# Kernel tuning notes

Hardware: AMD Instinct MI355X
Metric: run time of the kernel (lower is better)

The kernel has to match this reference:

```python
import jax, jax.numpy as jnp
import numpy as np

N_NODES = 50000
N_EDGES = 800000
IN_FEATS = 128
HIDDEN = 256
N_CLASSES = 64


def setup_inputs() -> dict:
    key = jax.random.key(0)
    ks = jax.random.split(key, 16)
    def w(k, shape, fan_in):
        return jax.random.normal(k, shape, dtype=jnp.float32) * (1.0 / np.sqrt(fan_in))
    inp = {
        "x": jax.random.normal(ks[0], (N_NODES, IN_FEATS), dtype=jnp.float32),
        "edge_src": jax.random.randint(ks[1], (N_EDGES,), 0, N_NODES, dtype=jnp.int32),
        "edge_dst": jax.random.randint(ks[2], (N_EDGES,), 0, N_NODES, dtype=jnp.int32),
        # layer 0: in_feats -> hidden
        "W0s": w(ks[3], (IN_FEATS, HIDDEN), IN_FEATS),
        "W0n": w(ks[4], (IN_FEATS, HIDDEN), IN_FEATS),
        "b0": jnp.zeros((HIDDEN,), dtype=jnp.float32),
        # layer 1: hidden -> hidden
        "W1s": w(ks[5], (HIDDEN, HIDDEN), HIDDEN),
        "W1n": w(ks[6], (HIDDEN, HIDDEN), HIDDEN),
        "b1": jnp.zeros((HIDDEN,), dtype=jnp.float32),
        # layer 2: hidden -> hidden (last conv also outputs hidden per source code)
        "W2s": w(ks[7], (HIDDEN, HIDDEN), HIDDEN),
        "W2n": w(ks[8], (HIDDEN, HIDDEN), HIDDEN),
        "b2": jnp.zeros((HIDDEN,), dtype=jnp.float32),
        # fc1: hidden -> n_classes
        "Wfc": w(ks[9], (HIDDEN, N_CLASSES), HIDDEN),
        "bfc": jnp.zeros((N_CLASSES,), dtype=jnp.float32),
    }
    return inp


def _sage_layer(h, src, dst, Ws, Wn, b):
    # mean-neighbor aggregation: segment-sum messages, divide by in-degree
    msg = h[src]  # [E, D] irregular gather
    agg = jax.ops.segment_sum(msg, dst, num_segments=N_NODES)  # [N, D]
    deg = jax.ops.segment_sum(jnp.ones_like(dst, dtype=h.dtype), dst, num_segments=N_NODES)
    h_neigh = agg / jnp.maximum(deg, 1.0)[:, None]
    # DGL SAGEConv (mean): fc_self(h) + fc_neigh(h_neigh) + bias
    return h @ Ws + h_neigh @ Wn + b


def reference(x, edge_src, edge_dst, W0s, W0n, b0, W1s, W1n, b1, W2s, W2n, b2, Wfc, bfc):
    # forward applies dropout (identity at eval) and NO activation between layers,
    # matching the original module's forward().
    h = _sage_layer(x, edge_src, edge_dst, W0s, W0n, b0)
    h = _sage_layer(h, edge_src, edge_dst, W1s, W1n, b1)
    h = _sage_layer(h, edge_src, edge_dst, W2s, W2n, b2)
    return h @ Wfc + bfc  # [N, n_classes]
```

## Files before the change

### kernel.cpp

```cpp
#include <hip/hip_runtime.h>

#define NN 50000
#define NE 800000
#define NE_HALF 400000
#define F_IN 128
#define HID 256
#define N_CLS 64
#define SCAN_BLOCKS ((NN + 255) / 256)
#define HEPT 4
#define HB2 ((NE + 256 * HEPT - 1) / (256 * HEPT))
#define HBH ((NE_HALF + 256 * HEPT - 1) / (256 * HEPT))
#define CF_BLOCKS 36
#define CL_BLOCKS 9
#define GA_BLOCKS ((NN + 127) / 128)
#define CROWS 515

typedef _Float16 half8 __attribute__((ext_vector_type(8)));
typedef float f32x4 __attribute__((ext_vector_type(4)));

__device__ __forceinline__ const float* virtC1_row(int r, const float* W0s,
                                                   const float* W0n, const float* b0) {
    if (r < 0) return nullptr;
    if (r < 128) return W0s + (size_t)r * 256;
    if (r < 256) return W0n + (size_t)(r - 128) * 256;
    if (r == 512) return b0;
    return nullptr;
}

__device__ __forceinline__ int shift_src(int r) {
    if (r >= 128 && r < 512) return r - 128;
    if (r == 513) return 512;
    if (r == 514) return 513;
    return -1;
}

__device__ __forceinline__ void compose_first_dev(
    int bx, const float* __restrict__ W0s, const float* __restrict__ W0n,
    const float* __restrict__ b0,
    const float* __restrict__ B1, const float* __restrict__ B2,
    const float* __restrict__ brow, float* __restrict__ C)
{
    __shared__ float As[64][17];
    __shared__ float Bs[16][64];
    const int tid = threadIdx.x;
    const int tx = tid & 15, ty = tid >> 4;
    const int row0 = (bx % 9) * 64;
    const int col0 = (bx / 9) * 64;
    const int lr = tid >> 2, lc = tid & 3;
    const int br = tid >> 4, bc = tid & 15;

    const int grow = row0 + lr;
    const int srcr0 = (grow < CROWS) ? grow : -1;
    const float* ap0 = virtC1_row(srcr0, W0s, W0n, b0);
    const float* ap1 = virtC1_row(shift_src(grow), W0s, W0n, b0);

    float acc[4][4] = {};

    float4 av = ap0 ? *(const float4*)(ap0 + lc * 4) : make_float4(0.f, 0.f, 0.f, 0.f);
    float4 bv = *(const float4*)(B1 + (size_t)br * 256 + col0 + bc * 4);

    for (int s = 0; s < 32; ++s) {
        As[lr][lc * 4 + 0] = av.x;
        As[lr][lc * 4 + 1] = av.y;
        As[lr][lc * 4 + 2] = av.z;
        As[lr][lc * 4 + 3] = av.w;
        *(float4*)&Bs[br][bc * 4] = bv;
        __syncthreads();
        if (s + 1 < 32) {
            int pass = (s + 1) >> 4;
            int k0 = ((s + 1) & 15) << 4;
            const float* ap = pass ? ap1 : ap0;
            const float* B = pass ? B2 : B1;
            av = ap ? *(const float4*)(ap + k0 + lc * 4) : make_float4(0.f, 0.f, 0.f, 0.f);
            bv = *(const float4*)(B + (size_t)(k0 + br) * 256 + col0 + bc * 4);
        }
        #pragma unroll
        for (int k = 0; k < 16; ++k) {
            float a[4];
            #pragma unroll
            for (int i = 0; i < 4; ++i) a[i] = As[ty * 4 + i][k];
            float4 bb = *(const float4*)&Bs[k][tx * 4];
            const float b[4] = {bb.x, bb.y, bb.z, bb.w};
            #pragma unroll
            for (int i = 0; i < 4; ++i)
                #pragma unroll
                for (int j = 0; j < 4; ++j)
                    acc[i][j] += a[i] * b[j];
        }
        __syncthreads();
    }

    #pragma unroll
    for (int i = 0; i < 4; ++i) {
        int r = row0 + ty * 4 + i;
        if (r < CROWS) {
            #pragma unroll
            for (int j = 0; j < 4; ++j) {
                float v = acc[i][j];
                if (r == 512) v += brow[col0 + tx * 4 + j];
                C[(size_t)r * 256 + col0 + tx * 4 + j] = v;
            }
        }
    }
}

__device__ __forceinline__ void compose_mid_dev(
    int bx, const float* __restrict__ A,
    const float* __restrict__ B1, const float* __restrict__ B2,
    const float* __restrict__ brow, float* __restrict__ C)
{
    __shared__ float As[64][17];
    __shared__ float Bs[16][64];
    const int tid = threadIdx.x;
    const int tx = tid & 15, ty = tid >> 4;
    const int row0 = (bx % 9) * 64;
    const int col0 = (bx / 9) * 64;
    const int lr = tid >> 2, lc = tid & 3;
    const int br = tid >> 4, bc = tid & 15;

    const int grow = row0 + lr;
    const int p0 = (grow < CROWS) ? grow : -1;
    const int p1 = shift_src(grow);

    float acc[4][4] = {};

    float4 av = (p0 >= 0) ? *(const float4*)(A + (size_t)p0 * 256 + lc * 4)
                          : make_float4(0.f, 0.f, 0.f, 0.f);
    float4 bv = *(const float4*)(B1 + (size_t)br * 256 + col0 + bc * 4);

    for (int s = 0; s < 32; ++s) {
        As[lr][lc * 4 + 0] = av.x;
        As[lr][lc * 4 + 1] = av.y;
        As[lr][lc * 4 + 2] = av.z;
        As[lr][lc * 4 + 3] = av.w;
        *(float4*)&Bs[br][bc * 4] = bv;
        __syncthreads();
        if (s + 1 < 32) {
            int pass = (s + 1) >> 4;
            int k0 = ((s + 1) & 15) << 4;
            int p = pass ? p1 : p0;
            const float* B = pass ? B2 : B1;
            av = (p >= 0) ? *(const float4*)(A + (size_t)p * 256 + k0 + lc * 4)
                          : make_float4(0.f, 0.f, 0.f, 0.f);
            bv = *(const float4*)(B + (size_t)(k0 + br) * 256 + col0 + bc * 4);
        }
        #pragma unroll
        for (int k = 0; k < 16; ++k) {
            float a[4];
            #pragma unroll
            for (int i = 0; i < 4; ++i) a[i] = As[ty * 4 + i][k];
            float4 bb = *(const float4*)&Bs[k][tx * 4];
            const float b[4] = {bb.x, bb.y, bb.z, bb.w};
            #pragma unroll
            for (int i = 0; i < 4; ++i)
                #pragma unroll
                for (int j = 0; j < 4; ++j)
                    acc[i][j] += a[i] * b[j];
        }
        __syncthreads();
    }

    #pragma unroll
    for (int i = 0; i < 4; ++i) {
        int r = row0 + ty * 4 + i;
        if (r < CROWS) {
            #pragma unroll
            for (int j = 0; j < 4; ++j) {
                float v = acc[i][j];
                if (r == 512) v += brow[col0 + tx * 4 + j];
                C[(size_t)r * 256 + col0 + tx * 4 + j] = v;
            }
        }
    }
}

__device__ __forceinline__ void compose_last_dev(
    int bx, const float* __restrict__ A, const float* __restrict__ B1,
    const float* __restrict__ brow, float* __restrict__ Vf, _Float16* __restrict__ BT)
{
    __shared__ float As[64][17];
    __shared__ float Bs[16][64];
    const int tid = threadIdx.x;
    const int tx = tid & 15, ty = tid >> 4;
    const int row0 = bx * 64;
    const int lr = tid >> 2, lc = tid & 3;
    const int br = tid >> 4, bc = tid & 15;

    const int grow = row0 + lr;
    const float* ap = (grow < CROWS) ? (A + (size_t)grow * 256) : nullptr;

    float acc[4][4] = {};

    float4 av = ap ? *(const float4*)(ap + lc * 4) : make_float4(0.f, 0.f, 0.f, 0.f);
    float4 bv = *(const float4*)(B1 + (size_t)br * 64 + bc * 4);

    for (int s = 0; s < 16; ++s) {
        As[lr][lc * 4 + 0] = av.x;
        As[lr][lc * 4 + 1] = av.y;
        As[lr][lc * 4 + 2] = av.z;
        As[lr][lc * 4 + 3] = av.w;
        *(float4*)&Bs[br][bc * 4] = bv;
        __syncthreads();
        if (s + 1 < 16) {
            int k0 = (s + 1) << 4;
            av = ap ? *(const float4*)(ap + k0 + lc * 4) : make_float4(0.f, 0.f, 0.f, 0.f);
            bv = *(const float4*)(B1 + (size_t)(k0 + br) * 64 + bc * 4);
        }
        #pragma unroll
        for (int k = 0; k < 16; ++k) {
            float a[4];
            #pragma unroll
            for (int i = 0; i < 4; ++i) a[i] = As[ty * 4 + i][k];
            float4 bb = *(const float4*)&Bs[k][tx * 4];
            const float b[4] = {bb.x, bb.y, bb.z, bb.w};
            #pragma unroll
            for (int i = 0; i < 4; ++i)
                #pragma unroll
                for (int j = 0; j < 4; ++j)
                    acc[i][j] += a[i] * b[j];
        }
        __syncthreads();
    }

    #pragma unroll
    for (int i = 0; i < 4; ++i) {
        int r = row0 + ty * 4 + i;
        if (r < CROWS) {
            #pragma unroll
            for (int j = 0; j < 4; ++j) {
                int c = tx * 4 + j;
                float v = acc[i][j];
                if (r == 512) v += brow[c];
                Vf[(size_t)r * 64 + c] = v;
                if (r < 512)
                    BT[(size_t)((r >> 7) * 64 + c) * 128 + (r & 127)] = (_Float16)v;
            }
        }
    }
}

__device__ __forceinline__ void hist_dev(int bx, int start, int count,
                                         const int* __restrict__ edst,
                                         int* __restrict__ cnt,
                                         unsigned short* __restrict__ rank) {
    int base = start + bx * (256 * HEPT) + threadIdx.x;
    int lim = start + count;
    int d[HEPT];
    #pragma unroll
    for (int k = 0; k < HEPT; ++k) {
        int e = base + k * 256;
        d[k] = (e < lim) ? edst[e] : -1;
    }
    #pragma unroll
    for (int k = 0; k < HEPT; ++k) {
        int e = base + k * 256;
        if (d[k] >= 0) rank[e] = (unsigned short)atomicAdd(&cnt[d[k]], 1);
    }
}

__device__ __forceinline__ void scan_block_sums_dev(const int* __restrict__ cnt,
                                                    int* __restrict__ blockSums, int n, int bx) {
    __shared__ int s[256];
    int t = threadIdx.x;
    int i = bx * 256 + t;
    s[t] = (i < n) ? cnt[i] : 0;
    __syncthreads();
    for (int off = 128; off > 0; off >>= 1) {
        if (t < off) s[t] += s[t + off];
        __syncthreads();
    }
    if (t == 0) blockSums[bx] = s[0];
}

__device__ __forceinline__ void scan_final2_dev(const int* __restrict__ cnt,
                                                const int* __restrict__ blockSums,
                                                int* __restrict__ offs,
                                                float* __restrict__ dinv, int n, int bx) {
    __shared__ int s[256];
    __shared__ int base_sh;
    int t = threadIdx.x;
    s[t] = (t < SCAN_BLOCKS) ? blockSums[t] : 0;
    __syncthreads();
    for (int off = 1; off < 256; off <<= 1) {
        int v = (t >= off) ? s[t - off] : 0;
        __syncthreads();
        s[t] += v;
        __syncthreads();
    }
    if (t == 0) base_sh = (bx > 0) ? s[bx - 1] : 0;
    __syncthreads();
    int base = base_sh;
    __syncthreads();
    int i = bx * 256 + t;
    int v = (i < n) ? cnt[i] : 0;
    s[t] = v;
    __syncthreads();
    for (int off = 1; off < 256; off <<= 1) {
        int u = (t >= off) ? s[t - off] : 0;
        __syncthreads();
        s[t] += u;
        __syncthreads();
    }
    if (i < n) {
        offs[i] = base + s[t] - v;
        dinv[i] = 1.0f / (float)max(v, 1);
    }
    if (i == n - 1) offs[n] = base + s[t];
}

__device__ __forceinline__ void gemm_y_dev(
    int bx, int by,
    const float* __restrict__ X, const _Float16* __restrict__ BT,
    _Float16* __restrict__ Y, _Float16* __restrict__ Tc, int N)
{
    constexpr int LP = 40;
    __shared__ _Float16 As[128 * LP];
    __shared__ _Float16 Bs[128 * LP];

    const int tid = threadIdx.x;
    const int wave = tid >> 6;
    const int lane = tid & 63;
    const int l15 = lane & 15;
    const int quad = lane >> 4;
    const int wrow = wave >> 1;
    const int wcol = wave & 1;
    const int m_base = wrow * 64;
    const int n_base = wcol * 64;

    const int row0 = bx * 128;
    const int col0 = by * 128;

    f32x4 acc[4][4] = {};

    for (int k0 = 0; k0 < 128; k0 += 32) {
        #pragma unroll
        for (int r = 0; r < 2; ++r) {
            int idx = r * 256 + tid;
            int row = idx >> 2, ch = idx & 3;
            int gr = row0 + row; if (gr > N - 1) gr = N - 1;
            const float* ap = X + (size_t)gr * 128 + k0 + ch * 8;
            float4 f0 = *(const float4*)ap;
            float4 f1 = *(const float4*)(ap + 4);
            half8 v = { (_Float16)f0.x, (_Float16)f0.y, (_Float16)f0.z, (_Float16)f0.w,
                        (_Float16)f1.x, (_Float16)f1.y, (_Float16)f1.z, (_Float16)f1.w };
            *(half8*)&As[row * LP + ch * 8] = v;
        }
        #pragma unroll
        for (int r = 0; r < 2; ++r) {
            int idx = r * 256 + tid;
            int row = idx >> 2, ch = idx & 3;
            *(half8*)&Bs[row * LP + ch * 8] =
                *(const half8*)(BT + (size_t)(col0 + row) * 128 + k0 + ch * 8);
        }
        __syncthreads();
        half8 af[4], bf[4];
        #pragma unroll
        for (int i = 0; i < 4; ++i)
            af[i] = *(const half8*)&As[(m_base + i * 16 + l15) * LP + quad * 8];
        #pragma unroll
        for (int j = 0; j < 4; ++j)
            bf[j] = *(const half8*)&Bs[(n_base + j * 16 + l15) * LP + quad * 8];
        #pragma unroll
        for (int i = 0; i < 4; ++i)
            #pragma unroll
            for (int j = 0; j < 4; ++j)
                acc[i][j] = __builtin_amdgcn_mfma_f32_16x16x32_f16(af[i], bf[j], acc[i][j], 0, 0, 0);
        __syncthreads();
    }

    #pragma unroll
    for (int i = 0; i < 4; ++i) {
        #pragma unroll
        for (int j = 0; j < 4; ++j) {
            int col = col0 + n_base + j * 16 + l15;
            #pragma unroll
            for (int r = 0; r < 4; ++r) {
                int row = row0 + m_base + i * 16 + quad * 4 + r;
                if (row < N) {
                    _Float16 v = (_Float16)acc[i][j][r];
                    Y[(size_t)row * 256 + col] = v;
                    if (col >= 192) Tc[(size_t)row * 64 + (col - 192)] = v;
                }
            }
        }
    }
}

__global__ __launch_bounds__(256) void k_composeF_hist(
    const int* __restrict__ edst, int* __restrict__ cnt, unsigned short* __restrict__ rank,
    const float* __restrict__ W0s, const float* __restrict__ W0n, const float* __restrict__ b0,
    const float* __restrict__ W1s, const float* __restrict__ W1n, const float* __restrict__ b1,
    float* __restrict__ C2)
{
    if (blockIdx.x < CF_BLOCKS) {
        compose_first_dev(blockIdx.x, W0s, W0n, b0, W1s, W1n, b1, C2);
    } else {
        hist_dev(blockIdx.x - CF_BLOCKS, 0, NE_HALF, edst, cnt, rank);
    }
}

__global__ __launch_bounds__(256) void k_composeM_hist2(
    const int* __restrict__ edst, int* __restrict__ cnt, unsigned short* __restrict__ rank,
    const float* __restrict__ C2,
    const float* __restrict__ W2s, const float* __restrict__ W2n, const float* __restrict__ b2,
    float* __restrict__ C3)
{
    if (blockIdx.x < CF_BLOCKS) compose_mid_dev(blockIdx.x, C2, W2s, W2n, b2, C3);
    else hist_dev(blockIdx.x - CF_BLOCKS, NE_HALF, NE - NE_HALF, edst, cnt, rank);
}

__global__ __launch_bounds__(256) void k_composeL_scanA(
    const int* __restrict__ cnt, int* __restrict__ blockSums,
    const float* __restrict__ C3, const float* __restrict__ Wfc, const float* __restrict__ bfc,
    float* __restrict__ Vf, _Float16* __restrict__ BT)
{
    if (blockIdx.x < CL_BLOCKS) compose_last_dev(blockIdx.x, C3, Wfc, bfc, Vf, BT);
    else scan_block_sums_dev(cnt, blockSums, NN, blockIdx.x - CL_BLOCKS);
}

__global__ __launch_bounds__(256) void k_gemmA_scanF(
    const int* __restrict__ cnt, const int* __restrict__ blockSums,
    int* __restrict__ offs, float* __restrict__ dinv,
    const float* __restrict__ X, const _Float16* __restrict__ BT,
    _Float16* __restrict__ Y, _Float16* __restrict__ Tc)
{
    if (blockIdx.x < GA_BLOCKS) gemm_y_dev(blockIdx.x, 0, X, BT, Y, Tc, NN);
    else scan_final2_dev(cnt, blockSums, offs, dinv, NN, blockIdx.x - GA_BLOCKS);
}

__global__ __launch_bounds__(256) void k_gemmB_place(
    const int* __restrict__ esrc, const int* __restrict__ edst,
    const unsigned short* __restrict__ rank, const int* __restrict__ offs,
    unsigned short* __restrict__ csr,
    const float* __restrict__ X, const _Float16* __restrict__ BT,
    _Float16* __restrict__ Y, _Float16* __restrict__ Tc)
{
    if (blockIdx.x < GA_BLOCKS) {
        gemm_y_dev(blockIdx.x, 1, X, BT, Y, Tc, NN);
    } else {
        int base = (blockIdx.x - GA_BLOCKS) * (256 * HEPT) + threadIdx.x;
        int d[HEPT], s[HEPT], r[HEPT];
        #pragma unroll
        for (int k = 0; k < HEPT; ++k) {
            int e = base + k * 256;
            if (e < NE) { d[k] = edst[e]; s[k] = esrc[e]; r[k] = rank[e]; }
            else d[k] = -1;
        }
        #pragma unroll
        for (int k = 0; k < HEPT; ++k) {
            if (d[k] >= 0) csr[offs[d[k]] + r[k]] = (unsigned short)s[k];
        }
    }
}

template <bool OUT_F32>
__global__ __launch_bounds__(256) void gather64(
    const _Float16* __restrict__ Tin,
    const unsigned short* __restrict__ csr, const int* __restrict__ offs,
    const float* __restrict__ dinv,
    const _Float16* __restrict__ Yadd,
    const float* __restrict__ cvec,
    void* __restrict__ Tout, int N)
{
    int node = blockIdx.x * 32 + (threadIdx.x >> 3);
    int lane = threadIdx.x & 7;
    if (node >= N) return;
    int beg = offs[node], end = offs[node + 1];
    float acc[8] = {};
    int e = beg;
    for (; e + 7 < end; e += 8) {
        int s0 = csr[e], s1 = csr[e + 1], s2 = csr[e + 2], s3 = csr[e + 3];
        int s4 = csr[e + 4], s5 = csr[e + 5], s6 = csr[e + 6], s7 = csr[e + 7];
        half8 v0 = *(const half8*)(Tin + (size_t)s0 * 64 + lane * 8);
        half8 v1 = *(const half8*)(Tin + (size_t)s1 * 64 + lane * 8);
        half8 v2 = *(const half8*)(Tin + (size_t)s2 * 64 + lane * 8);
        half8 v3 = *(const half8*)(Tin + (size_t)s3 * 64 + lane * 8);
        half8 v4 = *(const half8*)(Tin + (size_t)s4 * 64 + lane * 8);
        half8 v5 = *(const half8*)(Tin + (size_t)s5 * 64 + lane * 8);
        half8 v6 = *(const half8*)(Tin + (size_t)s6 * 64 + lane * 8);
        half8 v7 = *(const half8*)(Tin + (size_t)s7 * 64 + lane * 8);
        #pragma unroll
        for (int j = 0; j < 8; ++j)
            acc[j] += (((float)v0[j] + (float)v1[j]) + ((float)v2[j] + (float)v3[j]))
                    + (((float)v4[j] + (float)v5[j]) + ((float)v6[j] + (float)v7[j]));
    }
    for (; e + 3 < end; e += 4) {
        int s0 = csr[e], s1 = csr[e + 1], s2 = csr[e + 2], s3 = csr[e + 3];
        half8 v0 = *(const half8*)(Tin + (size_t)s0 * 64 + lane * 8);
        half8 v1 = *(const half8*)(Tin + (size_t)s1 * 64 + lane * 8);
        half8 v2 = *(const half8*)(Tin + (size_t)s2 * 64 + lane * 8);
        half8 v3 = *(const half8*)(Tin + (size_t)s3 * 64 + lane * 8);
        #pragma unroll
        for (int j = 0; j < 8; ++j)
            acc[j] += ((float)v0[j] + (float)v1[j]) + ((float)v2[j] + (float)v3[j]);
    }
    for (; e < end; ++e) {
        half8 v = *(const half8*)(Tin + (size_t)csr[e] * 64 + lane * 8);
        #pragma unroll
        for (int j = 0; j < 8; ++j) acc[j] += (float)v[j];
    }
    float sc = dinv[node];
    half8 y = *(const half8*)(Yadd + (size_t)node * 256 + lane * 8);
    if (OUT_F32) {
        float* o = (float*)Tout + (size_t)node * 64 + lane * 8;
        float4 o0, o1;
        o0.x = acc[0] * sc + (float)y[0] + cvec[lane * 8 + 0];
        o0.y = acc[1] * sc + (float)y[1] + cvec[lane * 8 + 1];
        o0.z = acc[2] * sc + (float)y[2] + cvec[lane * 8 + 2];
        o0.w = acc[3] * sc + (float)y[3] + cvec[lane * 8 + 3];
        o1.x = acc[4] * sc + (float)y[4] + cvec[lane * 8 + 4];
        o1.y = acc[5] * sc + (float)y[5] + cvec[lane * 8 + 5];
        o1.z = acc[6] * sc + (float)y[6] + cvec[lane * 8 + 6];
        o1.w = acc[7] * sc + (float)y[7] + cvec[lane * 8 + 7];
        *(float4*)o = o0;
        *(float4*)(o + 4) = o1;
    } else {
        half8 o;
        #pragma unroll
        for (int j = 0; j < 8; ++j)
            o[j] = (_Float16)(acc[j] * sc + (float)y[j] + cvec[lane * 8 + j]);
        *(half8*)((_Float16*)Tout + (size_t)node * 64 + lane * 8) = o;
    }
}

extern "C" void kernel_launch(void* const* d_in, const int* in_sizes, int n_in,
                              void* d_out, int out_size, void* d_ws, size_t ws_size,
                              hipStream_t stream) {
    const float* x    = (const float*)d_in[0];
    const int*   esrc = (const int*)d_in[1];
    const int*   edst = (const int*)d_in[2];
    const float* W0s  = (const float*)d_in[3];
    const float* W0n  = (const float*)d_in[4];
    const float* b0   = (const float*)d_in[5];
    const float* W1s  = (const float*)d_in[6];
    const float* W1n  = (const float*)d_in[7];
    const float* b1   = (const float*)d_in[8];
    const float* W2s  = (const float*)d_in[9];
    const float* W2n  = (const float*)d_in[10];
    const float* b2   = (const float*)d_in[11];
    const float* Wfc  = (const float*)d_in[12];
    const float* bfc  = (const float*)d_in[13];
    float* out = (float*)d_out;

    _Float16* Y   = (_Float16*)d_ws;
    _Float16* Ta  = Y + (size_t)NN * 256;
    _Float16* Tb  = Ta + (size_t)NN * 64;
    _Float16* Tc  = Tb + (size_t)NN * 64;
    _Float16* BT  = Tc + (size_t)NN * 64;
    float* C2     = (float*)(BT + 256 * 128);
    float* C3     = C2 + CROWS * 256;
    float* Vf     = C3 + CROWS * 256;
    float* dinv   = Vf + CROWS * 64;
    int* cnt      = (int*)(dinv + NN);
    int* offs     = cnt + NN;
    int* blockSums = offs + NN + 1;
    unsigned short* rank = (unsigned short*)(blockSums + SCAN_BLOCKS);
    unsigned short* csr  = rank + NE;

    hipMemsetAsync(cnt, 0, (size_t)NN * sizeof(int), stream);

    k_composeF_hist<<<CF_BLOCKS + HBH, 256, 0, stream>>>(
        edst, cnt, rank, W0s, W0n, b0, W1s, W1n, b1, C2);

    k_composeM_hist2<<<CF_BLOCKS + HBH, 256, 0, stream>>>(
        edst, cnt, rank, C2, W2s, W2n, b2, C3);

    k_composeL_scanA<<<CL_BLOCKS + SCAN_BLOCKS, 256, 0, stream>>>(
        cnt, blockSums, C3, Wfc, bfc, Vf, BT);

    k_gemmA_scanF<<<GA_BLOCKS + SCAN_BLOCKS, 256, 0, stream>>>(
        cnt, blockSums, offs, dinv, x, BT, Y, Tc);

    k_gemmB_place<<<GA_BLOCKS + HB2, 256, 0, stream>>>(
        esrc, edst, rank, offs, csr, x, BT, Y, Tc);

    const int ggrid = (NN + 31) / 32;
    gather64<false><<<ggrid, 256, 0, stream>>>(
        Tc, csr, offs, dinv, Y + 128, Vf + (size_t)514 * 64, (void*)Ta, NN);
    gather64<false><<<ggrid, 256, 0, stream>>>(
        Ta, csr, offs, dinv, Y + 64, Vf + (size_t)513 * 64, (void*)Tb, NN);
    gather64<true><<<ggrid, 256, 0, stream>>>(
        Tb, csr, offs, dinv, Y, Vf + (size_t)512 * 64, (void*)out, NN);
}
```

Baseline: 260.3 us.

## Reschedule fused kernels so first gather overlaps the GEMM half and histogram runs once

The stage schedule is reorganised. The full edge histogram now runs in the first kernel, and the scan moves earlier alongside the compose kernels. The GEMM half that writes Tc runs together with CSR placement. The other GEMM half is co-launched with the first gather, which removes one launch. The histogram's edges-per-thread value also drops from 4 to 2. The co-scheduled gather reads Tc and writes Ta while the gemm blocks in the same launch write different Y columns, so correctness depends on that column split holding.

```diff
diff --git a/kernel.cpp b/kernel.cpp
--- a/kernel.cpp
+++ b/kernel.cpp
@@ -2,17 +2,16 @@
 
 #define NN 50000
 #define NE 800000
-#define NE_HALF 400000
 #define F_IN 128
 #define HID 256
 #define N_CLS 64
 #define SCAN_BLOCKS ((NN + 255) / 256)
-#define HEPT 4
-#define HB2 ((NE + 256 * HEPT - 1) / (256 * HEPT))
-#define HBH ((NE_HALF + 256 * HEPT - 1) / (256 * HEPT))
+#define HEPT 2
+#define HBF ((NE + 256 * HEPT - 1) / (256 * HEPT))
 #define CF_BLOCKS 36
 #define CL_BLOCKS 9
 #define GA_BLOCKS ((NN + 127) / 128)
+#define GG_BLOCKS ((NN + 31) / 32)
 #define CROWS 515
 
 typedef _Float16 half8 __attribute__((ext_vector_type(8)));
@@ -239,17 +238,15 @@
     }
 }
 
-__device__ __forceinline__ void hist_dev(int bx, int start, int count,
-                                         const int* __restrict__ edst,
+__device__ __forceinline__ void hist_dev(int bx, const int* __restrict__ edst,
                                          int* __restrict__ cnt,
                                          unsigned short* __restrict__ rank) {
-    int base = start + bx * (256 * HEPT) + threadIdx.x;
-    int lim = start + count;
+    int base = bx * (256 * HEPT) + threadIdx.x;
     int d[HEPT];
     #pragma unroll
     for (int k = 0; k < HEPT; ++k) {
         int e = base + k * 256;
-        d[k] = (e < lim) ? edst[e] : -1;
+        d[k] = (e < NE) ? edst[e] : -1;
     }
     #pragma unroll
     for (int k = 0; k < HEPT; ++k) {
@@ -386,85 +383,16 @@
     }
 }
 
-__global__ __launch_bounds__(256) void k_composeF_hist(
-    const int* __restrict__ edst, int* __restrict__ cnt, unsigned short* __restrict__ rank,
-    const float* __restrict__ W0s, const float* __restrict__ W0n, const float* __restrict__ b0,
-    const float* __restrict__ W1s, const float* __restrict__ W1n, const float* __restrict__ b1,
-    float* __restrict__ C2)
-{
-    if (blockIdx.x < CF_BLOCKS) {
-        compose_first_dev(blockIdx.x, W0s, W0n, b0, W1s, W1n, b1, C2);
-    } else {
-        hist_dev(blockIdx.x - CF_BLOCKS, 0, NE_HALF, edst, cnt, rank);
-    }
-}
-
-__global__ __launch_bounds__(256) void k_composeM_hist2(
-    const int* __restrict__ edst, int* __restrict__ cnt, unsigned short* __restrict__ rank,
-    const float* __restrict__ C2,
-    const float* __restrict__ W2s, const float* __restrict__ W2n, const float* __restrict__ b2,
-    float* __restrict__ C3)
-{
-    if (blockIdx.x < CF_BLOCKS) compose_mid_dev(blockIdx.x, C2, W2s, W2n, b2, C3);
-    else hist_dev(blockIdx.x - CF_BLOCKS, NE_HALF, NE - NE_HALF, edst, cnt, rank);
-}
-
-__global__ __launch_bounds__(256) void k_composeL_scanA(
-    const int* __restrict__ cnt, int* __restrict__ blockSums,
-    const float* __restrict__ C3, const float* __restrict__ Wfc, const float* __restrict__ bfc,
-    float* __restrict__ Vf, _Float16* __restrict__ BT)
-{
-    if (blockIdx.x < CL_BLOCKS) compose_last_dev(blockIdx.x, C3, Wfc, bfc, Vf, BT);
-    else scan_block_sums_dev(cnt, blockSums, NN, blockIdx.x - CL_BLOCKS);
-}
-
-__global__ __launch_bounds__(256) void k_gemmA_scanF(
-    const int* __restrict__ cnt, const int* __restrict__ blockSums,
-    int* __restrict__ offs, float* __restrict__ dinv,
-    const float* __restrict__ X, const _Float16* __restrict__ BT,
-    _Float16* __restrict__ Y, _Float16* __restrict__ Tc)
-{
-    if (blockIdx.x < GA_BLOCKS) gemm_y_dev(blockIdx.x, 0, X, BT, Y, Tc, NN);
-    else scan_final2_dev(cnt, blockSums, offs, dinv, NN, blockIdx.x - GA_BLOCKS);
-}
-
-__global__ __launch_bounds__(256) void k_gemmB_place(
-    const int* __restrict__ esrc, const int* __restrict__ edst,
-    const unsigned short* __restrict__ rank, const int* __restrict__ offs,
-    unsigned short* __restrict__ csr,
-    const float* __restrict__ X, const _Float16* __restrict__ BT,
-    _Float16* __restrict__ Y, _Float16* __restrict__ Tc)
-{
-    if (blockIdx.x < GA_BLOCKS) {
-        gemm_y_dev(blockIdx.x, 1, X, BT, Y, Tc, NN);
-    } else {
-        int base = (blockIdx.x - GA_BLOCKS) * (256 * HEPT) + threadIdx.x;
-        int d[HEPT], s[HEPT], r[HEPT];
-        #pragma unroll
-        for (int k = 0; k < HEPT; ++k) {
-            int e = base + k * 256;
-            if (e < NE) { d[k] = edst[e]; s[k] = esrc[e]; r[k] = rank[e]; }
-            else d[k] = -1;
-        }
-        #pragma unroll
-        for (int k = 0; k < HEPT; ++k) {
-            if (d[k] >= 0) csr[offs[d[k]] + r[k]] = (unsigned short)s[k];
-        }
-    }
-}
-
 template <bool OUT_F32>
-__global__ __launch_bounds__(256) void gather64(
+__device__ __forceinline__ void gather_node_dev(
+    int node, int lane,
     const _Float16* __restrict__ Tin,
     const unsigned short* __restrict__ csr, const int* __restrict__ offs,
     const float* __restrict__ dinv,
     const _Float16* __restrict__ Yadd,
     const float* __restrict__ cvec,
-    void* __restrict__ Tout, int N)
-{
-    int node = blockIdx.x * 32 + (threadIdx.x >> 3);
-    int lane = threadIdx.x & 7;
-    if (node >= N) return;
+    void* __restrict__ Tout)
+{
     int beg = offs[node], end = offs[node + 1];
     float acc[8] = {};
     int e = beg;
@@ -521,6 +449,97 @@
             o[j] = (_Float16)(acc[j] * sc + (float)y[j] + cvec[lane * 8 + j]);
         *(half8*)((_Float16*)Tout + (size_t)node * 64 + lane * 8) = o;
     }
+}
+
+__global__ __launch_bounds__(256) void k_composeF_hist(
+    const int* __restrict__ edst, int* __restrict__ cnt, unsigned short* __restrict__ rank,
+    const float* __restrict__ W0s, const float* __restrict__ W0n, const float* __restrict__ b0,
+    const float* __restrict__ W1s, const float* __restrict__ W1n, const float* __restrict__ b1,
+    float* __restrict__ C2)
+{
+    if (blockIdx.x < CF_BLOCKS) {
+        compose_first_dev(blockIdx.x, W0s, W0n, b0, W1s, W1n, b1, C2);
+    } else {
+        hist_dev(blockIdx.x - CF_BLOCKS, edst, cnt, rank);
+    }
+}
+
+__global__ __launch_bounds__(256) void k_composeM_scanA(
+    const int* __restrict__ cnt, int* __restrict__ blockSums,
+    const float* __restrict__ C2,
+    const float* __restrict__ W2s, const float* __restrict__ W2n, const float* __restrict__ b2,
+    float* __restrict__ C3)
+{
+    if (blockIdx.x < CF_BLOCKS) compose_mid_dev(blockIdx.x, C2, W2s, W2n, b2, C3);
+    else scan_block_sums_dev(cnt, blockSums, NN, blockIdx.x - CF_BLOCKS);
+}
+
+__global__ __launch_bounds__(256) void k_composeL_scanF(
+    const int* __restrict__ cnt, const int* __restrict__ blockSums,
+    int* __restrict__ offs, float* __restrict__ dinv,
+    const float* __restrict__ C3, const float* __restrict__ Wfc, const float* __restrict__ bfc,
+    float* __restrict__ Vf, _Float16* __restrict__ BT)
+{
+    if (blockIdx.x < CL_BLOCKS) compose_last_dev(blockIdx.x, C3, Wfc, bfc, Vf, BT);
+    else scan_final2_dev(cnt, blockSums, offs, dinv, NN, blockIdx.x - CL_BLOCKS);
+}
+
+__global__ __launch_bounds__(256) void k_gemmT_place(
+    const int* __restrict__ esrc, const int* __restrict__ edst,
+    const unsigned short* __restrict__ rank, const int* __restrict__ offs,
+    unsigned short* __restrict__ csr,
+    const float* __restrict__ X, const _Float16* __restrict__ BT,
+    _Float16* __restrict__ Y, _Float16* __restrict__ Tc)
+{
+    if (blockIdx.x < GA_BLOCKS) {
+        gemm_y_dev(blockIdx.x, 1, X, BT, Y, Tc, NN);
+    } else {
+        int base = (blockIdx.x - GA_BLOCKS) * (256 * HEPT) + threadIdx.x;
+        int d[HEPT], s[HEPT], r[HEPT];
+        #pragma unroll
+        for (int k = 0; k < HEPT; ++k) {
+            int e = base + k * 256;
+            if (e < NE) { d[k] = edst[e]; s[k] = esrc[e]; r[k] = rank[e]; }
+            else d[k] = -1;
+        }
+        #pragma unroll
+        for (int k = 0; k < HEPT; ++k) {
+            if (d[k] >= 0) csr[offs[d[k]] + r[k]] = (unsigned short)s[k];
+        }
+    }
+}
+
+__global__ __launch_bounds__(256) void k_gemmA_gather1(
+    const float* __restrict__ X, const _Float16* __restrict__ BT,
+    _Float16* __restrict__ Y, _Float16* __restrict__ Tc,
+    const unsigned short* __restrict__ csr, const int* __restrict__ offs,
+    const float* __restrict__ dinv, const float* __restrict__ Vf,
+    _Float16* __restrict__ Ta)
+{
+    if (blockIdx.x < GA_BLOCKS) {
+        gemm_y_dev(blockIdx.x, 0, X, BT, Y, Tc, NN);
+    } else {
+        int node = (blockIdx.x - GA_BLOCKS) * 32 + (threadIdx.x >> 3);
+        int lane = threadIdx.x & 7;
+        if (node < NN)
+            gather_node_dev<false>(node, lane, Tc, csr, offs, dinv,
+                                   Y + 128, Vf + (size_t)514 * 64, (void*)Ta);
+    }
+}
+
+template <bool OUT_F32>
+__global__ __launch_bounds__(256) void gather64(
+    const _Float16* __restrict__ Tin,
+    const unsigned short* __restrict__ csr, const int* __restrict__ offs,
+    const float* __restrict__ dinv,
+    const _Float16* __restrict__ Yadd,
+    const float* __restrict__ cvec,
+    void* __restrict__ Tout, int N)
+{
+    int node = blockIdx.x * 32 + (threadIdx.x >> 3);
+    int lane = threadIdx.x & 7;
+    if (node >= N) return;
+    gather_node_dev<OUT_F32>(node, lane, Tin, csr, offs, dinv, Yadd, cvec, Tout);
 }
 
 extern "C" void kernel_launch(void* const* d_in, const int* in_sizes, int n_in,
@@ -559,26 +578,23 @@
 
     hipMemsetAsync(cnt, 0, (size_t)NN * sizeof(int), stream);
 
-    k_composeF_hist<<<CF_BLOCKS + HBH, 256, 0, stream>>>(
+    k_composeF_hist<<<CF_BLOCKS + HBF, 256, 0, stream>>>(
         edst, cnt, rank, W0s, W0n, b0, W1s, W1n, b1, C2);
 
-    k_composeM_hist2<<<CF_BLOCKS + HBH, 256, 0, stream>>>(
-        edst, cnt, rank, C2, W2s, W2n, b2, C3);
-
-    k_composeL_scanA<<<CL_BLOCKS + SCAN_BLOCKS, 256, 0, stream>>>(
-        cnt, blockSums, C3, Wfc, bfc, Vf, BT);
-
-    k_gemmA_scanF<<<GA_BLOCKS + SCAN_BLOCKS, 256, 0, stream>>>(
-        cnt, blockSums, offs, dinv, x, BT, Y, Tc);
-
-    k_gemmB_place<<<GA_BLOCKS + HB2, 256, 0, stream>>>(
+    k_composeM_scanA<<<CF_BLOCKS + SCAN_BLOCKS, 256, 0, stream>>>(
+        cnt, blockSums, C2, W2s, W2n, b2, C3);
+
+    k_composeL_scanF<<<CL_BLOCKS + SCAN_BLOCKS, 256, 0, stream>>>(
+        cnt, blockSums, offs, dinv, C3, Wfc, bfc, Vf, BT);
+
+    k_gemmT_place<<<GA_BLOCKS + HBF, 256, 0, stream>>>(
         esrc, edst, rank, offs, csr, x, BT, Y, Tc);
 
-    const int ggrid = (NN + 31) / 32;
-    gather64<false><<<ggrid, 256, 0, stream>>>(
-        Tc, csr, offs, dinv, Y + 128, Vf + (size_t)514 * 64, (void*)Ta, NN);
-    gather64<false><<<ggrid, 256, 0, stream>>>(
+    k_gemmA_gather1<<<GA_BLOCKS + GG_BLOCKS, 256, 0, stream>>>(
+        x, BT, Y, Tc, csr, offs, dinv, Vf, Ta);
+
+    gather64<false><<<GG_BLOCKS, 256, 0, stream>>>(
         Ta, csr, offs, dinv, Y + 64, Vf + (size_t)513 * 64, (void*)Tb, NN);
-    gather64<true><<<ggrid, 256, 0, stream>>>(
+    gather64<true><<<GG_BLOCKS, 256, 0, stream>>>(
         Tb, csr, offs, dinv, Y, Vf + (size_t)512 * 64, (void*)out, NN);
 }
```

Result: slower. 272.2 us (+4.6%).
